# Kernel optimization log

Measured on AMD Instinct MI355X. Metric: run time of the kernel, lower is better.

## Reference

```python
import jax, jax.numpy as jnp
import numpy as np

D = 2048
H = 32
EPS = 1e-5


def _ln(z, scale, bias):
    m = jnp.mean(z, axis=-1, keepdims=True)
    v = jnp.mean(jnp.square(z - m), axis=-1, keepdims=True)
    return (z - m) / jnp.sqrt(v + EPS) * scale + bias


def setup_inputs() -> dict:
    key = jax.random.key(0)
    ks = jax.random.split(key, 12)
    B, S = 4, 1024
    s = 0.02
    return {
        "x": jax.random.normal(ks[0], (B, S, D), jnp.float32),
        "Wq": jax.random.normal(ks[1], (D, D), jnp.float32) * s,
        "Wk": jax.random.normal(ks[2], (D, D), jnp.float32) * s,
        "Wv": jax.random.normal(ks[3], (D, D), jnp.float32) * s,
        "ln1_scale": jnp.ones((D,), jnp.float32) + jax.random.normal(ks[4], (D,), jnp.float32) * s,
        "ln1_bias": jax.random.normal(ks[5], (D,), jnp.float32) * s,
        "ln2_scale": jnp.ones((D,), jnp.float32) + jax.random.normal(ks[6], (D,), jnp.float32) * s,
        "ln2_bias": jax.random.normal(ks[7], (D,), jnp.float32) * s,
        "ff1_w": jax.random.normal(ks[8], (D, D), jnp.float32) * s,
        "ff1_b": jax.random.normal(ks[9], (D,), jnp.float32) * s,
        "ff2_w": jax.random.normal(ks[10], (D, D), jnp.float32) * s,
        "ff2_b": jax.random.normal(ks[11], (D,), jnp.float32) * s,
    }


def reference(x, Wq, Wk, Wv, ln1_scale, ln1_bias, ln2_scale, ln2_bias,
              ff1_w, ff1_b, ff2_w, ff2_b):
    B, S, _ = x.shape
    hd = D // H
    residual = x
    h = _ln(x, ln1_scale, ln1_bias)
    # QKV projections (no bias, per source)
    q = (h @ Wq).reshape(B, S, H, hd).transpose(0, 2, 1, 3)  # [B,H,S,hd]
    k = (h @ Wk).reshape(B, S, H, hd).transpose(0, 2, 1, 3)
    v = (h @ Wv).reshape(B, S, H, hd).transpose(0, 2, 1, 3)
    # NOTE: source scales by input_size**0.5 (full D), not head_dim
    scores = jnp.einsum('bhqd,bhkd->bhqk', q, k) / jnp.sqrt(jnp.float32(D))
    attn_probs = jax.nn.softmax(scores, axis=-1)  # [B,H,S,S]
    # attended_values is computed in the source but NEVER used (source bug, kept faithful)
    _attended = jnp.einsum('bhqk,bhkd->bhqd', attn_probs, v)
    del _attended
    x2 = h + residual  # source: x += residual, where x is LN1 output
    h2 = _ln(x2, ln2_scale, ln2_bias)
    ff = jnp.maximum(h2 @ ff1_w + ff1_b, 0.0) @ ff2_w + ff2_b
    out = ff + x2
    return out, attn_probs
```

## Files before the change

### kernel.cpp

```cpp
#include <hip/hip_runtime.h>
#include <math.h>


typedef unsigned short u16;
typedef u16    u16x4  __attribute__((ext_vector_type(4)));
typedef u16    u16x8  __attribute__((ext_vector_type(8)));
typedef __bf16 bf16x8 __attribute__((ext_vector_type(8)));
typedef float  f32x4  __attribute__((ext_vector_type(4)));

#define MFMA16(a, b, c) __builtin_amdgcn_mfma_f32_16x16x32_bf16((a), (b), (c), 0, 0, 0)

__device__ __forceinline__ u16 f2bf(float f) {
  unsigned u = __builtin_bit_cast(unsigned, f);
  u += 0x7fffu + ((u >> 16) & 1u);
  return (u16)(u >> 16);
}

__device__ __forceinline__ void gload_lds16(const u16* g, u16* l) {
  __builtin_amdgcn_global_load_lds(
      (const __attribute__((address_space(1))) unsigned int*)g,
      (__attribute__((address_space(3))) unsigned int*)l, 16, 0, 0);
}

__global__ __launch_bounds__(256) void transpose_cast4(
    const float* __restrict__ W0, const float* __restrict__ W1,
    const float* __restrict__ W2, const float* __restrict__ W3,
    u16* __restrict__ dst) {
  __shared__ u16 tile[64][65];
  const int z = blockIdx.z;
  const float* W = (z == 0) ? W0 : (z == 1) ? W1 : (z == 2) ? W2 : W3;
  u16* WT = dst + (size_t)z * 2048 * 2048;
  const int n0 = blockIdx.x * 64, k0 = blockIdx.y * 64;
  const int c = threadIdx.x & 63, rb = threadIdx.x >> 6;
#pragma unroll
  for (int i = 0; i < 16; i++) {
    int r = rb + i * 4;
    tile[r][c] = f2bf(W[(size_t)(k0 + r) * 2048 + n0 + c]);
  }
  __syncthreads();
#pragma unroll
  for (int i = 0; i < 16; i++) {
    int r = rb + i * 4;
    WT[(size_t)(n0 + r) * 2048 + k0 + c] = tile[c][r];
  }
}

__global__ __launch_bounds__(256) void ln_fused(
    const float* __restrict__ x,
    const float* __restrict__ s1, const float* __restrict__ b1,
    const float* __restrict__ s2, const float* __restrict__ b2,
    u16* __restrict__ h_bf, float* __restrict__ x2o, u16* __restrict__ h2_bf) {
  const int wid = threadIdx.x >> 6, lane = threadIdx.x & 63;
  const size_t rbase = (size_t)(blockIdx.x * 4 + wid) * 2048;

  float v[32];
#pragma unroll
  for (int i = 0; i < 8; i++)
    *(float4*)&v[i * 4] = *(const float4*)(x + rbase + i * 256 + lane * 4);

  float s = 0.f;
#pragma unroll
  for (int i = 0; i < 32; i++) s += v[i];
#pragma unroll
  for (int off = 32; off; off >>= 1) s += __shfl_xor(s, off, 64);
  const float m1 = s * (1.f / 2048.f);

  float ss = 0.f;
#pragma unroll
  for (int i = 0; i < 32; i++) { float d = v[i] - m1; ss += d * d; }
#pragma unroll
  for (int off = 32; off; off >>= 1) ss += __shfl_xor(ss, off, 64);
  const float r1 = rsqrtf(ss * (1.f / 2048.f) + 1e-5f);

  float xx[32];
#pragma unroll
  for (int i = 0; i < 8; i++) {
    const int c = i * 256 + lane * 4;
    float4 w4 = *(const float4*)(s1 + c);
    float4 b4 = *(const float4*)(b1 + c);
    u16x4 hv;
#pragma unroll
    for (int j = 0; j < 4; j++) {
      float hh = (v[i * 4 + j] - m1) * r1 * (&w4.x)[j] + (&b4.x)[j];
      xx[i * 4 + j] = hh + v[i * 4 + j];
      hv[j] = f2bf(hh);
    }
    *(u16x4*)(h_bf + rbase + c) = hv;
    *(float4*)(x2o + rbase + c) = *(float4*)&xx[i * 4];
  }

  s = 0.f;
#pragma unroll
  for (int i = 0; i < 32; i++) s += xx[i];
#pragma unroll
  for (int off = 32; off; off >>= 1) s += __shfl_xor(s, off, 64);
  const float m2 = s * (1.f / 2048.f);

  ss = 0.f;
#pragma unroll
  for (int i = 0; i < 32; i++) { float d = xx[i] - m2; ss += d * d; }
#pragma unroll
  for (int off = 32; off; off >>= 1) ss += __shfl_xor(ss, off, 64);
  const float r2 = rsqrtf(ss * (1.f / 2048.f) + 1e-5f);

#pragma unroll
  for (int i = 0; i < 8; i++) {
    const int c = i * 256 + lane * 4;
    float4 w4 = *(const float4*)(s2 + c);
    float4 b4 = *(const float4*)(b2 + c);
    u16x4 hv;
#pragma unroll
    for (int j = 0; j < 4; j++)
      hv[j] = f2bf((xx[i * 4 + j] - m2) * r2 * (&w4.x)[j] + (&b4.x)[j]);
    *(u16x4*)(h2_bf + rbase + c) = hv;
  }
}

template <int N, int BIAS, int RELU, int RESID, int OUTBF>
__global__ __launch_bounds__(256) void gemm_bf16(
    const u16* __restrict__ A, const u16* __restrict__ BT,
    const float* __restrict__ bias, const float* __restrict__ resid,
    void* __restrict__ Cout) {
  constexpr int K = 2048, BK = 64;
  __shared__ u16 As[128 * BK];
  __shared__ u16 Bs[128 * BK];
  const int tid = threadIdx.x;
  const int row0 = blockIdx.y * 128, col0 = blockIdx.x * 128;
  const int wid = tid >> 6, lane = tid & 63, lr = lane & 15, quad = lane >> 4;
  const int wr0 = (wid >> 1) * 64, wc0 = (wid & 1) * 64;
  const int srow = lane >> 3;
  const int scol = (lane & 7) * 8;

  f32x4 acc[4][4];
#pragma unroll
  for (int i = 0; i < 4; i++)
#pragma unroll
    for (int j = 0; j < 4; j++) acc[i][j] = (f32x4){0.f, 0.f, 0.f, 0.f};

  const u16* gA = A + (size_t)(row0 + srow) * K + scol;
  const u16* gB = BT + (size_t)(col0 + srow) * K + scol;

  for (int k0 = 0; k0 < K; k0 += BK) {
    if (k0) __syncthreads();
#pragma unroll
    for (int i = 0; i < 4; i++) {
      const int rg = i * 32 + wid * 8;
      gload_lds16(gA + (size_t)rg * K + k0, &As[rg * BK]);
      gload_lds16(gB + (size_t)rg * K + k0, &Bs[rg * BK]);
    }
    __syncthreads();

#pragma unroll
    for (int kk = 0; kk < 2; kk++) {
      bf16x8 af[4], bfr[4];
#pragma unroll
      for (int i = 0; i < 4; i++)
        af[i] = *(const bf16x8*)&As[(wr0 + i * 16 + lr) * BK + kk * 32 + quad * 8];
#pragma unroll
      for (int j = 0; j < 4; j++)
        bfr[j] = *(const bf16x8*)&Bs[(wc0 + j * 16 + lr) * BK + kk * 32 + quad * 8];
#pragma unroll
      for (int i = 0; i < 4; i++)
#pragma unroll
        for (int j = 0; j < 4; j++) acc[i][j] = MFMA16(af[i], bfr[j], acc[i][j]);
    }
  }

#pragma unroll
  for (int i = 0; i < 4; i++) {
#pragma unroll
    for (int r = 0; r < 4; r++) {
      const int row = row0 + wr0 + i * 16 + quad * 4 + r;
#pragma unroll
      for (int j = 0; j < 4; j++) {
        const int col = col0 + wc0 + j * 16 + lr;
        float v = acc[i][j][r];
        if (BIAS) v += bias[col];
        if (RELU) v = fmaxf(v, 0.f);
        if (RESID) v += resid[(size_t)row * N + col];
        if (OUTBF)
          ((u16*)Cout)[(size_t)row * N + col] = f2bf(v);
        else
          ((float*)Cout)[(size_t)row * N + col] = v;
      }
    }
  }
}

__global__ __launch_bounds__(256) void attn_kernel(const u16* __restrict__ qk,
                                                   float* __restrict__ probs) {
  __shared__ float sc[16 * 1024];
  const int tid = threadIdx.x, wid = tid >> 6, lane = tid & 63;
  const int lr = lane & 15, quad = lane >> 4;
  const int q0 = blockIdx.x * 16, h = blockIdx.y, b = blockIdx.z;

  const size_t qbase = (size_t)(b * 1024 + q0 + lr) * 4096 + h * 64 + quad * 8;
  const bf16x8 a0 = *(const bf16x8*)(qk + qbase);
  const bf16x8 a1 = *(const bf16x8*)(qk + qbase + 32);
  const float scale = 0.022097086912079608f;

  for (int t = 0; t < 16; t++) {
    const int c0 = wid * 256 + t * 16;
    const size_t kbase = (size_t)(b * 1024 + c0 + lr) * 4096 + 2048 + h * 64 + quad * 8;
    const bf16x8 b0 = *(const bf16x8*)(qk + kbase);
    const bf16x8 b1 = *(const bf16x8*)(qk + kbase + 32);
    f32x4 acc = (f32x4){0.f, 0.f, 0.f, 0.f};
    acc = MFMA16(a0, b0, acc);
    acc = MFMA16(a1, b1, acc);
#pragma unroll
    for (int r = 0; r < 4; r++) sc[(quad * 4 + r) * 1024 + c0 + lr] = acc[r] * scale;
  }
  __syncthreads();

#pragma unroll
  for (int rr = 0; rr < 4; rr++) {
    const int row = wid * 4 + rr;
    float vals[16];
#pragma unroll
    for (int i = 0; i < 4; i++)
      *(float4*)&vals[i * 4] = *(const float4*)&sc[row * 1024 + i * 256 + lane * 4];
    float mx = -1e30f;
#pragma unroll
    for (int i = 0; i < 16; i++) mx = fmaxf(mx, vals[i]);
#pragma unroll
    for (int off = 32; off; off >>= 1) mx = fmaxf(mx, __shfl_xor(mx, off, 64));
    float sum = 0.f;
#pragma unroll
    for (int i = 0; i < 16; i++) {
      vals[i] = __expf(vals[i] - mx);
      sum += vals[i];
    }
#pragma unroll
    for (int off = 32; off; off >>= 1) sum += __shfl_xor(sum, off, 64);
    const float inv = 1.f / sum;
    float* pr = probs + (size_t)((b * 32 + h) * 1024 + q0 + row) * 1024;
#pragma unroll
    for (int i = 0; i < 4; i++) {
      float4 o;
#pragma unroll
      for (int j = 0; j < 4; j++) (&o.x)[j] = vals[i * 4 + j] * inv;
      *(float4*)&pr[i * 256 + lane * 4] = o;
    }
  }
}

extern "C" void kernel_launch(void* const* d_in, const int* in_sizes, int n_in,
                              void* d_out, int out_size, void* d_ws, size_t ws_size,
                              hipStream_t stream) {
  const float* x = (const float*)d_in[0];
  const float* Wq = (const float*)d_in[1];
  const float* Wk = (const float*)d_in[2];
  const float* ln1s = (const float*)d_in[4];
  const float* ln1b = (const float*)d_in[5];
  const float* ln2s = (const float*)d_in[6];
  const float* ln2b = (const float*)d_in[7];
  const float* f1w = (const float*)d_in[8];
  const float* f1b = (const float*)d_in[9];
  const float* f2w = (const float*)d_in[10];
  const float* f2b = (const float*)d_in[11];

  char* p = (char*)d_ws;
  const size_t WSZ = (size_t)2048 * 2048 * 2;
  const size_t ASZ = (size_t)4096 * 2048 * 2;
  u16* WqkT = (u16*)p; p += 2 * WSZ;
  u16* F1T = (u16*)p; p += WSZ;
  u16* F2T = (u16*)p; p += WSZ;
  u16* h_bf = (u16*)p; p += ASZ;
  u16* h2_bf = (u16*)p; p += ASZ;
  u16* qk_bf = (u16*)p; p += 2 * ASZ;
  u16* a1_bf = (u16*)p; p += ASZ;
  float* x2 = (float*)p; p += (size_t)4096 * 2048 * 4;

  float* out = (float*)d_out;
  float* probs = out + (size_t)4096 * 2048;

  transpose_cast4<<<dim3(32, 32, 4), 256, 0, stream>>>(Wq, Wk, f1w, f2w, WqkT);

  ln_fused<<<1024, 256, 0, stream>>>(x, ln1s, ln1b, ln2s, ln2b, h_bf, x2, h2_bf);

  gemm_bf16<4096, 0, 0, 0, 1><<<dim3(32, 32), 256, 0, stream>>>(
      h_bf, WqkT, nullptr, nullptr, qk_bf);

  attn_kernel<<<dim3(64, 32, 4), 256, 0, stream>>>(qk_bf, probs);

  const dim3 gg(16, 32);
  gemm_bf16<2048, 1, 1, 0, 1><<<gg, 256, 0, stream>>>(h2_bf, F1T, f1b, nullptr, a1_bf);
  gemm_bf16<2048, 1, 0, 1, 0><<<gg, 256, 0, stream>>>(a1_bf, F2T, f2b, x2, out);
}
```

Before: 985.5 us.

## Merge weight transpose with LN kernel, swizzle attention LDS, nontemporal prob stores

```diff
diff --git a/kernel.cpp b/kernel.cpp
--- a/kernel.cpp
+++ b/kernel.cpp
@@ -22,36 +22,42 @@
       (__attribute__((address_space(3))) unsigned int*)l, 16, 0, 0);
 }
 
-__global__ __launch_bounds__(256) void transpose_cast4(
+__device__ __forceinline__ void nt_store4(float* p, f32x4 v) {
+  __builtin_nontemporal_store(v, (f32x4*)p);
+}
+
+__global__ __launch_bounds__(256) void prep_kernel(
     const float* __restrict__ W0, const float* __restrict__ W1,
     const float* __restrict__ W2, const float* __restrict__ W3,
-    u16* __restrict__ dst) {
-  __shared__ u16 tile[64][65];
-  const int z = blockIdx.z;
-  const float* W = (z == 0) ? W0 : (z == 1) ? W1 : (z == 2) ? W2 : W3;
-  u16* WT = dst + (size_t)z * 2048 * 2048;
-  const int n0 = blockIdx.x * 64, k0 = blockIdx.y * 64;
-  const int c = threadIdx.x & 63, rb = threadIdx.x >> 6;
-#pragma unroll
-  for (int i = 0; i < 16; i++) {
-    int r = rb + i * 4;
-    tile[r][c] = f2bf(W[(size_t)(k0 + r) * 2048 + n0 + c]);
-  }
-  __syncthreads();
-#pragma unroll
-  for (int i = 0; i < 16; i++) {
-    int r = rb + i * 4;
-    WT[(size_t)(n0 + r) * 2048 + k0 + c] = tile[c][r];
-  }
-}
-
-__global__ __launch_bounds__(256) void ln_fused(
+    u16* __restrict__ dst,
     const float* __restrict__ x,
     const float* __restrict__ s1, const float* __restrict__ b1,
     const float* __restrict__ s2, const float* __restrict__ b2,
     u16* __restrict__ h_bf, float* __restrict__ x2o, u16* __restrict__ h2_bf) {
+  __shared__ u16 tile[64][65];
+  const int bx = blockIdx.x;
+  if (bx < 4096) {
+    const int z = bx >> 10, rem = bx & 1023;
+    const float* W = (z == 0) ? W0 : (z == 1) ? W1 : (z == 2) ? W2 : W3;
+    u16* WT = dst + (size_t)z * 2048 * 2048;
+    const int n0 = (rem & 31) * 64, k0 = (rem >> 5) * 64;
+    const int c = threadIdx.x & 63, rb = threadIdx.x >> 6;
+#pragma unroll
+    for (int i = 0; i < 16; i++) {
+      int r = rb + i * 4;
+      tile[r][c] = f2bf(W[(size_t)(k0 + r) * 2048 + n0 + c]);
+    }
+    __syncthreads();
+#pragma unroll
+    for (int i = 0; i < 16; i++) {
+      int r = rb + i * 4;
+      WT[(size_t)(n0 + r) * 2048 + k0 + c] = tile[c][r];
+    }
+    return;
+  }
+
   const int wid = threadIdx.x >> 6, lane = threadIdx.x & 63;
-  const size_t rbase = (size_t)(blockIdx.x * 4 + wid) * 2048;
+  const size_t rbase = (size_t)((bx - 4096) * 4 + wid) * 2048;
 
   float v[32];
 #pragma unroll
@@ -199,6 +205,7 @@
   const bf16x8 a1 = *(const bf16x8*)(qk + qbase + 32);
   const float scale = 0.022097086912079608f;
 
+  const int ssw = quad & 1;
   for (int t = 0; t < 16; t++) {
     const int c0 = wid * 256 + t * 16;
     const size_t kbase = (size_t)(b * 1024 + c0 + lr) * 4096 + 2048 + h * 64 + quad * 8;
@@ -207,18 +214,22 @@
     f32x4 acc = (f32x4){0.f, 0.f, 0.f, 0.f};
     acc = MFMA16(a0, b0, acc);
     acc = MFMA16(a1, b1, acc);
-#pragma unroll
-    for (int r = 0; r < 4; r++) sc[(quad * 4 + r) * 1024 + c0 + lr] = acc[r] * scale;
+    const int pc = ((wid * 16 + t) ^ ssw) * 16 + lr;
+#pragma unroll
+    for (int r = 0; r < 4; r++) sc[(quad * 4 + r) * 1024 + pc] = acc[r] * scale;
   }
   __syncthreads();
 
+  const int rsw = wid & 1;
 #pragma unroll
   for (int rr = 0; rr < 4; rr++) {
     const int row = wid * 4 + rr;
     float vals[16];
 #pragma unroll
-    for (int i = 0; i < 4; i++)
-      *(float4*)&vals[i * 4] = *(const float4*)&sc[row * 1024 + i * 256 + lane * 4];
+    for (int i = 0; i < 4; i++) {
+      const int pidx = (i * 16 + ((lane >> 2) ^ rsw)) * 16 + (lane & 3) * 4;
+      *(f32x4*)&vals[i * 4] = *(const f32x4*)&sc[row * 1024 + pidx];
+    }
     float mx = -1e30f;
 #pragma unroll
     for (int i = 0; i < 16; i++) mx = fmaxf(mx, vals[i]);
@@ -236,10 +247,10 @@
     float* pr = probs + (size_t)((b * 32 + h) * 1024 + q0 + row) * 1024;
 #pragma unroll
     for (int i = 0; i < 4; i++) {
-      float4 o;
-#pragma unroll
-      for (int j = 0; j < 4; j++) (&o.x)[j] = vals[i * 4 + j] * inv;
-      *(float4*)&pr[i * 256 + lane * 4] = o;
+      f32x4 o;
+#pragma unroll
+      for (int j = 0; j < 4; j++) o[j] = vals[i * 4 + j] * inv;
+      nt_store4(&pr[i * 256 + lane * 4], o);
     }
   }
 }
@@ -274,9 +285,9 @@
   float* out = (float*)d_out;
   float* probs = out + (size_t)4096 * 2048;
 
-  transpose_cast4<<<dim3(32, 32, 4), 256, 0, stream>>>(Wq, Wk, f1w, f2w, WqkT);
-
-  ln_fused<<<1024, 256, 0, stream>>>(x, ln1s, ln1b, ln2s, ln2b, h_bf, x2, h2_bf);
+  prep_kernel<<<5120, 256, 0, stream>>>(Wq, Wk, f1w, f2w, WqkT,
+                                        x, ln1s, ln1b, ln2s, ln2b,
+                                        h_bf, x2, h2_bf);
 
   gemm_bf16<4096, 0, 0, 0, 1><<<dim3(32, 32), 256, 0, stream>>>(
       h_bf, WqkT, nullptr, nullptr, qk_bf);
```

Result: faster. 893.0 us (-9.4%).
